# Kernel tuning notes

Hardware: AMD Instinct MI355X
Metric: run time of the kernel (lower is better)

Reference implementation:

```python
import jax, jax.numpy as jnp
import numpy as np

B, V_PREV, V_NEXT = 1, 16384, 65536
F_IN, F_OUT = 512, 256
NNZ_UP, N_EDGE = 65536, 524288
EPS = 1e-5


def batch_spmm(row, col, val, m, x):
    # sparse [m, n] (COO row/col/val) @ dense x [B, n, d] -> [B, m, d]
    contrib = val[None, :, None] * x[:, col, :]          # [B, nnz, d]
    return jnp.zeros((x.shape[0], m, x.shape[2]), x.dtype).at[:, row, :].add(contrib)


def batchnorm(x, g, b):
    # BatchNorm1d in training mode: stats over (batch, node) per channel
    mu = jnp.mean(x, axis=(0, 1), keepdims=True)
    var = jnp.var(x, axis=(0, 1), keepdims=True)
    return (x - mu) * jax.lax.rsqrt(var + EPS) * g + b


def ecc(x, src, dst, w, Ui_W, Ui_b, Uj_W, Uj_b):
    # edge-conditioned graph conv: out_i = Ui(x_i) + sum_{(j->i)} w_e * Uj(x_j)
    n_nodes = x.shape[1]
    uj = x @ Uj_W + Uj_b                                  # [B, V, Fout]
    msg = w[None, :, None] * uj[:, src, :]                # [B, E, Fout]
    agg = jnp.zeros((x.shape[0], n_nodes, Uj_W.shape[1]), x.dtype).at[:, dst, :].add(msg)
    return x @ Ui_W + Ui_b + agg


def setup_inputs() -> dict:
    key = jax.random.key(0)
    ks = jax.random.split(key, 16)
    s_in = 1.0 / np.sqrt(F_IN)
    s_out = 1.0 / np.sqrt(F_OUT)
    p = {}
    p["x"] = jax.random.normal(ks[0], (B, V_PREV, F_IN), jnp.float32)
    p["up_row"] = jnp.arange(NNZ_UP, dtype=jnp.int32)
    p["up_col"] = jax.random.randint(ks[1], (NNZ_UP,), 0, V_PREV)
    p["up_val"] = jax.random.uniform(ks[2], (NNZ_UP,), jnp.float32)
    p["edge_src"] = jax.random.randint(ks[3], (N_EDGE,), 0, V_NEXT)
    p["edge_dst"] = jax.random.randint(ks[4], (N_EDGE,), 0, V_NEXT)
    p["adj_val"] = jax.random.uniform(ks[5], (N_EDGE,), jnp.float32)
    p["W_res"] = jax.random.normal(ks[6], (F_IN, F_OUT), jnp.float32) * s_in
    p["b_res"] = jnp.zeros((F_OUT,), jnp.float32)
    p["bn0_g"] = jnp.ones((F_IN,), jnp.float32)
    p["bn0_b"] = jnp.zeros((F_IN,), jnp.float32)
    p["bn1_g"] = jnp.ones((F_OUT,), jnp.float32)
    p["bn1_b"] = jnp.zeros((F_OUT,), jnp.float32)
    p["Ui0_W"] = jax.random.normal(ks[7], (F_IN, F_OUT), jnp.float32) * s_in
    p["Ui0_b"] = jnp.zeros((F_OUT,), jnp.float32)
    p["Uj0_W"] = jax.random.normal(ks[8], (F_IN, F_OUT), jnp.float32) * s_in
    p["Uj0_b"] = jnp.zeros((F_OUT,), jnp.float32)
    p["Ui1_W"] = jax.random.normal(ks[9], (F_OUT, F_OUT), jnp.float32) * s_out
    p["Ui1_b"] = jnp.zeros((F_OUT,), jnp.float32)
    p["Uj1_W"] = jax.random.normal(ks[10], (F_OUT, F_OUT), jnp.float32) * s_out
    p["Uj1_b"] = jnp.zeros((F_OUT,), jnp.float32)
    return p


def reference(x, up_row, up_col, up_val, edge_src, edge_dst, adj_val,
              W_res, b_res, bn0_g, bn0_b, bn1_g, bn1_b,
              Ui0_W, Ui0_b, Uj0_W, Uj0_b, Ui1_W, Ui1_b, Uj1_W, Uj1_b):
    # residual branch: sparse upsample then 1x1 conv (= linear over channels)
    residual = batch_spmm(up_row, up_col, up_val, V_NEXT, x)      # [B, V_NEXT, F_IN]
    residual = residual @ W_res + b_res                           # [B, V_NEXT, F_OUT]
    # main branch
    out = jax.nn.relu(batchnorm(x, bn0_g, bn0_b))                 # [B, V_PREV, F_IN]
    out = batch_spmm(up_row, up_col, up_val, V_NEXT, out)         # [B, V_NEXT, F_IN]
    out = ecc(out, edge_src, edge_dst, adj_val, Ui0_W, Ui0_b, Uj0_W, Uj0_b)
    out = jax.nn.relu(batchnorm(out, bn1_g, bn1_b))
    out = ecc(out, edge_src, edge_dst, adj_val, Ui1_W, Ui1_b, Uj1_W, Uj1_b)
    return out + residual
```

## Files before the change

kernel.cpp:

```cpp
#include <hip/hip_runtime.h>

#define V_PREV 16384
#define V_NEXT 65536
#define F_IN   512
#define F_OUT  256
#define NNZ_UP 65536
#define N_EDGE 524288

using f32x4 = __attribute__((ext_vector_type(4))) float;
using bfrag = __attribute__((ext_vector_type(8))) short;

__device__ __forceinline__ ushort f2bf(float f) {
    union { float f; unsigned u; } v; v.f = f;
    unsigned r = (v.u + 0x7FFFu + ((v.u >> 16) & 1u)) >> 16;
    return (ushort)r;
}
__device__ __forceinline__ float bf2f(ushort h) {
    union { unsigned u; float f; } v; v.u = ((unsigned)h) << 16; return v.f;
}

__global__ void prep_all_kernel(const float* __restrict__ Wres,
                                const float* __restrict__ Ui0W, const float* __restrict__ Uj0W,
                                const float* __restrict__ Ui1W, const float* __restrict__ Uj1W,
                                const float* __restrict__ Ui1b, const float* __restrict__ bres,
                                const int* __restrict__ up_row, const int* __restrict__ up_col,
                                const float* __restrict__ up_val,
                                ushort* __restrict__ WresT, ushort* __restrict__ W0t,
                                ushort* __restrict__ W1cat, float* __restrict__ biasUi,
                                int* __restrict__ colof, float* __restrict__ valof,
                                int* __restrict__ zeroBase)
{
    int b = blockIdx.x, t = threadIdx.x;
    if (b < 1024) {
        int i = b * 256 + t;
        if (i < 256 * 512) {
            int n = i / 512, k = i % 512;
            WresT[i] = f2bf(Wres[k * 256 + n]);
            W1cat[i] = f2bf(k < 256 ? Ui1W[k * 256 + n] : Uj1W[(k - 256) * 256 + n]);
        }
        {
            int n = i / 512, k = i % 512;
            W0t[i] = f2bf(n < 256 ? Uj0W[k * 256 + n] : Ui0W[k * 256 + (n - 256)]);
        }
        if (i < 256) biasUi[i] = Ui1b[i] + bres[i];
    } else if (b < 1280) {
        int k = (b - 1024) * 256 + t;
        int r = up_row[k];
        colof[r] = up_col[k];
        valof[r] = up_val[k];
    } else {
        int i = (b - 1280) * 256 + t;
        zeroBase[i] = 0;
    }
}

__global__ void hist_bn0_kernel(const int* __restrict__ dst, const float* __restrict__ adjv,
                                int* __restrict__ cnt, float* __restrict__ sumA,
                                const float* __restrict__ x,
                                float* __restrict__ psum0, float* __restrict__ psq0)
{
    int b = blockIdx.x, t = threadIdx.x;
    if (b < 2048) {
        int e = b * 256 + t;
        int d = dst[e];
        atomicAdd(&cnt[d], 1);
        atomicAdd(&sumA[d], adjv[e]);
    } else {
        int blk = b - 2048;
        float s0 = 0, s1 = 0, q0 = 0, q1 = 0;
        for (int r = 0; r < 128; r++) {
            size_t base = ((size_t)blk * 128 + r) * 512;
            float a = x[base + t], bb = x[base + t + 256];
            s0 += a; q0 += a * a; s1 += bb; q1 += bb * bb;
        }
        psum0[blk * 512 + t] = s0; psum0[blk * 512 + t + 256] = s1;
        psq0 [blk * 512 + t] = q0; psq0 [blk * 512 + t + 256] = q1;
    }
}

__global__ void scan_block_kernel(const int* __restrict__ cnt, int* __restrict__ offs,
                                  int* __restrict__ bsum)
{
    __shared__ int buf[2][256];
    int t = threadIdx.x;
    int i = blockIdx.x * 256 + t;
    int v = cnt[i];
    int p = 0;
    buf[0][t] = v;
    __syncthreads();
    for (int d = 1; d < 256; d <<= 1) {
        int nv = buf[p][t] + ((t >= d) ? buf[p][t - d] : 0);
        buf[p ^ 1][t] = nv;
        p ^= 1;
        __syncthreads();
    }
    int incl = buf[p][t];
    offs[i] = incl - v;
    if (t == 255) bsum[blockIdx.x] = incl;
}

__global__ void add_offs_bnfin_kernel(int* __restrict__ offs, const int* __restrict__ bsum,
                                      int* __restrict__ cursor,
                                      const float* __restrict__ psum0, const float* __restrict__ psq0,
                                      const float* __restrict__ g0, const float* __restrict__ b0,
                                      float* __restrict__ sc0, float* __restrict__ sh0)
{
    int b = blockIdx.x, t = threadIdx.x;
    if (b < 256) {
        __shared__ int buf[2][256];
        int v = bsum[t];
        int p = 0;
        buf[0][t] = v;
        __syncthreads();
        for (int d = 1; d < 256; d <<= 1) {
            int nv = buf[p][t] + ((t >= d) ? buf[p][t - d] : 0);
            buf[p ^ 1][t] = nv;
            p ^= 1;
            __syncthreads();
        }
        int excl = buf[p][b] - bsum[b];
        int i = b * 256 + t;
        int o = offs[i] + excl;
        offs[i] = o;
        cursor[i] = o;
    } else {
        int vb = b - 256;
        int gw = (vb * 256 + t) >> 6;
        int lane = t & 63;
        float s = 0, q = 0;
        for (int i = lane; i < 128; i += 64) {
            s += psum0[(size_t)i * 512 + gw];
            q += psq0 [(size_t)i * 512 + gw];
        }
#pragma unroll
        for (int d = 32; d > 0; d >>= 1) {
            s += __shfl_xor(s, d);
            q += __shfl_xor(q, d);
        }
        if (lane == 0) {
            float m = s * (1.0f / V_PREV);
            float v = q * (1.0f / V_PREV) - m * m;
            float r = rsqrtf(v + 1e-5f);
            float scale = r * g0[gw];
            sc0[gw] = scale;
            sh0[gw] = b0[gw] - m * scale;
        }
    }
}

__global__ void fill_kernel(const int* __restrict__ src, const int* __restrict__ dst,
                            const float* __restrict__ adjv,
                            const int* __restrict__ colof, const float* __restrict__ valof,
                            int* __restrict__ cursor,
                            int* __restrict__ srcsA, float* __restrict__ valsA,
                            int* __restrict__ srcs0, float* __restrict__ vals0)
{
    int e = blockIdx.x * blockDim.x + threadIdx.x;
    int d = dst[e];
    int s = src[e];
    float a = adjv[e];
    int p = atomicAdd(&cursor[d], 1);
    srcsA[p] = s;
    valsA[p] = a;
    srcs0[p] = colof[s];
    vals0[p] = a * valof[s];
}

__global__ void bn_finish_kernel(const float* __restrict__ psum, const float* __restrict__ psq,
                                 int nblocks, int C, float invN,
                                 const float* __restrict__ g, const float* __restrict__ b,
                                 float* __restrict__ sc, float* __restrict__ sh)
{
    int gw = (blockIdx.x * blockDim.x + threadIdx.x) >> 6;
    int lane = threadIdx.x & 63;
    if (gw >= C) return;
    float s = 0, q = 0;
    for (int i = lane; i < nblocks; i += 64) {
        s += psum[(size_t)i * C + gw];
        q += psq [(size_t)i * C + gw];
    }
#pragma unroll
    for (int d = 32; d > 0; d >>= 1) {
        s += __shfl_xor(s, d);
        q += __shfl_xor(q, d);
    }
    if (lane == 0) {
        float m = s * invN;
        float v = q * invN - m * m;
        float r = rsqrtf(v + 1e-5f);
        float scale = r * g[gw];
        sc[gw] = scale;
        sh[gw] = b[gw] - m * scale;
    }
}

__global__ __launch_bounds__(256)
void gemm0_fused_kernel(const float* __restrict__ x,
                        const ushort* __restrict__ WresT, const ushort* __restrict__ W0t,
                        const float* __restrict__ sc0, const float* __restrict__ sh0,
                        ushort* __restrict__ XW, ushort* __restrict__ XNJ,
                        ushort* __restrict__ XNI)
{
    __shared__ ushort As[128 * 32];
    __shared__ ushort Bs[128 * 32];
    __shared__ float s_sc[512], s_sh[512];

    const int tid = threadIdx.x;
    const int id   = blockIdx.x;
    const int xcd  = id & 7;
    const int rest = id >> 3;
    const int slot = rest / 6;
    const int bx   = rest - slot * 6;
    const int by   = slot * 8 + xcd;

    const bool bnmode = bx >= 2;
    const ushort* Bt = bnmode ? W0t : WresT;
    const int btrow = bnmode ? (bx - 2) * 128 : bx * 128;
    ushort* Cout = (bx < 2) ? XW : (bx < 4 ? XNJ : XNI);
    const int colbase = (bx & 1) * 128;
    const int tM = by * 128;

    for (int i = tid; i < 512; i += 256) { s_sc[i] = sc0[i]; s_sh[i] = sh0[i]; }
    __syncthreads();

    const int lane = tid & 63;
    const int wave = tid >> 6;
    const int wm = wave >> 1, wn = wave & 1;
    const int lr = lane & 15, lg = lane >> 4;

    const int ra = tid >> 1;
    const int ua = (tid & 1) * 2;
    const int rb = tid >> 2;
    const int ub = tid & 3;

    f32x4 acc[4][4] = {};

    for (int k0 = 0; k0 < 512; k0 += 32) {
        const float* xp = &x[(size_t)(tM + ra) * 512 + k0 + ua * 8];
        float4 f0 = *(const float4*)(xp);
        float4 f1 = *(const float4*)(xp + 4);
        float4 f2 = *(const float4*)(xp + 8);
        float4 f3 = *(const float4*)(xp + 12);
        float vv[16] = { f0.x,f0.y,f0.z,f0.w, f1.x,f1.y,f1.z,f1.w,
                         f2.x,f2.y,f2.z,f2.w, f3.x,f3.y,f3.z,f3.w };
        ushort hh[16];
        if (bnmode) {
#pragma unroll
            for (int j = 0; j < 16; j++) {
                int c = k0 + ua * 8 + j;
                hh[j] = f2bf(fmaxf(vv[j] * s_sc[c] + s_sh[c], 0.0f));
            }
        } else {
#pragma unroll
            for (int j = 0; j < 16; j++) hh[j] = f2bf(vv[j]);
        }
        *(uint4*)&As[ra * 32 + ((ua    ) ^ (ra & 3)) * 8] = *(uint4*)&hh[0];
        *(uint4*)&As[ra * 32 + ((ua + 1) ^ (ra & 3)) * 8] = *(uint4*)&hh[8];

#pragma unroll
        for (int i = 0; i < 2; i++) {
            int row = rb + i * 64;
            *(uint4*)&Bs[row * 32 + (ub ^ (row & 3)) * 8] =
                *(const uint4*)&Bt[(size_t)(btrow + row) * 512 + k0 + ub * 8];
        }
        __syncthreads();

        bfrag af[4], bfv[4];
#pragma unroll
        for (int mm = 0; mm < 4; mm++) {
            int row = wm * 64 + mm * 16 + lr;
            af[mm] = *(const bfrag*)&As[row * 32 + (lg ^ (row & 3)) * 8];
        }
#pragma unroll
        for (int nn = 0; nn < 4; nn++) {
            int row = wn * 64 + nn * 16 + lr;
            bfv[nn] = *(const bfrag*)&Bs[row * 32 + (lg ^ (row & 3)) * 8];
        }
#pragma unroll
        for (int mm = 0; mm < 4; mm++)
#pragma unroll
            for (int nn = 0; nn < 4; nn++)
                acc[mm][nn] = __builtin_amdgcn_mfma_f32_16x16x32_bf16(af[mm], bfv[nn], acc[mm][nn], 0, 0, 0);
        __syncthreads();
    }

#pragma unroll
    for (int mm = 0; mm < 4; mm++)
#pragma unroll
        for (int nn = 0; nn < 4; nn++)
#pragma unroll
            for (int r = 0; r < 4; r++) {
                int row = tM + wm * 64 + mm * 16 + lg * 4 + r;
                int col = colbase + wn * 64 + nn * 16 + lr;
                Cout[(size_t)row * 256 + col] = f2bf(acc[mm][nn][r]);
            }
}

__global__ __launch_bounds__(256)
void gather0_kernel(const int* __restrict__ offs, const int* __restrict__ cnt,
                    const int* __restrict__ srcs0, const float* __restrict__ vals0,
                    const int* __restrict__ colof, const float* __restrict__ valof,
                    const float* __restrict__ sumA,
                    const ushort* __restrict__ XNJ, const ushort* __restrict__ XNI,
                    const float* __restrict__ ui_b, const float* __restrict__ uj_b,
                    ushort* __restrict__ X1,
                    float* __restrict__ psum1s, float* __restrict__ psq1s)
{
    __shared__ float redS[4][256];
    __shared__ float redQ[4][256];

    int wave = threadIdx.x >> 6;
    int f = (threadIdx.x & 63) * 4;
    float ub0 = ui_b[f + 0], ub1 = ui_b[f + 1], ub2 = ui_b[f + 2], ub3 = ui_b[f + 3];
    float jb0 = uj_b[f + 0], jb1 = uj_b[f + 1], jb2 = uj_b[f + 2], jb3 = uj_b[f + 3];
    float ss0 = 0, ss1 = 0, ss2 = 0, ss3 = 0;
    float qq0 = 0, qq1 = 0, qq2 = 0, qq3 = 0;

    for (int it = 0; it < 8; it++) {
        int d = (blockIdx.x * 8 + it) * 4 + wave;
        int c = colof[d];
        float s = valof[d];
        float sA = sumA[d];
        ushort4 u = *(const ushort4*)&XNI[(size_t)c * 256 + f];
        const ushort* up = (const ushort*)&u;
        float a0 = ub0 + sA * jb0 + s * bf2f(up[0]);
        float a1 = ub1 + sA * jb1 + s * bf2f(up[1]);
        float a2 = ub2 + sA * jb2 + s * bf2f(up[2]);
        float a3 = ub3 + sA * jb3 + s * bf2f(up[3]);

        int st = offs[d], n = cnt[d];
        for (int e0 = 0; e0 < n; e0 += 4) {
            int   i0 = srcs0[st + e0];
            float w0 = vals0[st + e0];
            int i1 = 0, i2 = 0, i3 = 0;
            float w1 = 0, w2 = 0, w3 = 0;
            if (e0 + 1 < n) { i1 = srcs0[st + e0 + 1]; w1 = vals0[st + e0 + 1]; }
            if (e0 + 2 < n) { i2 = srcs0[st + e0 + 2]; w2 = vals0[st + e0 + 2]; }
            if (e0 + 3 < n) { i3 = srcs0[st + e0 + 3]; w3 = vals0[st + e0 + 3]; }
            ushort4 v0 = *(const ushort4*)&XNJ[(size_t)i0 * 256 + f];
            ushort4 v1 = *(const ushort4*)&XNJ[(size_t)i1 * 256 + f];
            ushort4 v2 = *(const ushort4*)&XNJ[(size_t)i2 * 256 + f];
            ushort4 v3 = *(const ushort4*)&XNJ[(size_t)i3 * 256 + f];
            const ushort* p0 = (const ushort*)&v0;
            const ushort* p1 = (const ushort*)&v1;
            const ushort* p2 = (const ushort*)&v2;
            const ushort* p3 = (const ushort*)&v3;
            a0 += w0 * bf2f(p0[0]) + w1 * bf2f(p1[0]) + w2 * bf2f(p2[0]) + w3 * bf2f(p3[0]);
            a1 += w0 * bf2f(p0[1]) + w1 * bf2f(p1[1]) + w2 * bf2f(p2[1]) + w3 * bf2f(p3[1]);
            a2 += w0 * bf2f(p0[2]) + w1 * bf2f(p1[2]) + w2 * bf2f(p2[2]) + w3 * bf2f(p3[2]);
            a3 += w0 * bf2f(p0[3]) + w1 * bf2f(p1[3]) + w2 * bf2f(p2[3]) + w3 * bf2f(p3[3]);
        }
        *(ushort4*)&X1[(size_t)d * 256 + f] =
            make_ushort4(f2bf(a0), f2bf(a1), f2bf(a2), f2bf(a3));
        ss0 += a0; ss1 += a1; ss2 += a2; ss3 += a3;
        qq0 += a0 * a0; qq1 += a1 * a1; qq2 += a2 * a2; qq3 += a3 * a3;
    }

    redS[wave][f + 0] = ss0; redS[wave][f + 1] = ss1;
    redS[wave][f + 2] = ss2; redS[wave][f + 3] = ss3;
    redQ[wave][f + 0] = qq0; redQ[wave][f + 1] = qq1;
    redQ[wave][f + 2] = qq2; redQ[wave][f + 3] = qq3;
    __syncthreads();
    int t = threadIdx.x;
    float ssum = redS[0][t] + redS[1][t] + redS[2][t] + redS[3][t];
    float sq   = redQ[0][t] + redQ[1][t] + redQ[2][t] + redQ[3][t];
    int slab = (blockIdx.x & 63) * 256 + t;
    atomicAdd(&psum1s[slab], ssum);
    atomicAdd(&psq1s[slab], sq);
}

__global__ __launch_bounds__(256)
void gather1G_kernel(const int* __restrict__ offs, const int* __restrict__ cnt,
                     const int* __restrict__ srcsA, const float* __restrict__ valsA,
                     const ushort* __restrict__ X1,
                     const float* __restrict__ sc1, const float* __restrict__ sh1,
                     ushort* __restrict__ G)
{
    int d = blockIdx.x * 4 + (threadIdx.x >> 6);
    int f = (threadIdx.x & 63) * 4;
    float4 sc = *(const float4*)&sc1[f];
    float4 sh = *(const float4*)&sh1[f];
    float a0 = 0, a1 = 0, a2 = 0, a3 = 0;

    int st = offs[d], n = cnt[d];
    for (int e0 = 0; e0 < n; e0 += 4) {
        int   i0 = srcsA[st + e0];
        float w0 = valsA[st + e0];
        int i1 = 0, i2 = 0, i3 = 0;
        float w1 = 0, w2 = 0, w3 = 0;
        if (e0 + 1 < n) { i1 = srcsA[st + e0 + 1]; w1 = valsA[st + e0 + 1]; }
        if (e0 + 2 < n) { i2 = srcsA[st + e0 + 2]; w2 = valsA[st + e0 + 2]; }
        if (e0 + 3 < n) { i3 = srcsA[st + e0 + 3]; w3 = valsA[st + e0 + 3]; }
        ushort4 v0 = *(const ushort4*)&X1[(size_t)i0 * 256 + f];
        ushort4 v1 = *(const ushort4*)&X1[(size_t)i1 * 256 + f];
        ushort4 v2 = *(const ushort4*)&X1[(size_t)i2 * 256 + f];
        ushort4 v3 = *(const ushort4*)&X1[(size_t)i3 * 256 + f];
        const ushort* p0 = (const ushort*)&v0;
        const ushort* p1 = (const ushort*)&v1;
        const ushort* p2 = (const ushort*)&v2;
        const ushort* p3 = (const ushort*)&v3;
        a0 += w0 * fmaxf(bf2f(p0[0]) * sc.x + sh.x, 0.0f)
            + w1 * fmaxf(bf2f(p1[0]) * sc.x + sh.x, 0.0f)
            + w2 * fmaxf(bf2f(p2[0]) * sc.x + sh.x, 0.0f)
            + w3 * fmaxf(bf2f(p3[0]) * sc.x + sh.x, 0.0f);
        a1 += w0 * fmaxf(bf2f(p0[1]) * sc.y + sh.y, 0.0f)
            + w1 * fmaxf(bf2f(p1[1]) * sc.y + sh.y, 0.0f)
            + w2 * fmaxf(bf2f(p2[1]) * sc.y + sh.y, 0.0f)
            + w3 * fmaxf(bf2f(p3[1]) * sc.y + sh.y, 0.0f);
        a2 += w0 * fmaxf(bf2f(p0[2]) * sc.z + sh.z, 0.0f)
            + w1 * fmaxf(bf2f(p1[2]) * sc.z + sh.z, 0.0f)
            + w2 * fmaxf(bf2f(p2[2]) * sc.z + sh.z, 0.0f)
            + w3 * fmaxf(bf2f(p3[2]) * sc.z + sh.z, 0.0f);
        a3 += w0 * fmaxf(bf2f(p0[3]) * sc.w + sh.w, 0.0f)
            + w1 * fmaxf(bf2f(p1[3]) * sc.w + sh.w, 0.0f)
            + w2 * fmaxf(bf2f(p2[3]) * sc.w + sh.w, 0.0f)
            + w3 * fmaxf(bf2f(p3[3]) * sc.w + sh.w, 0.0f);
    }
    *(ushort4*)&G[(size_t)d * 256 + f] =
        make_ushort4(f2bf(a0), f2bf(a1), f2bf(a2), f2bf(a3));
}

__global__ __launch_bounds__(512, 1)
void gemm_final_kernel(const ushort* __restrict__ X1, const ushort* __restrict__ G,
                       const ushort* __restrict__ W1cat,
                       const float* __restrict__ sc1, const float* __restrict__ sh1,
                       const float* __restrict__ biasUi, const float* __restrict__ uj1_b,
                       const float* __restrict__ sumA,
                       const int* __restrict__ colof, const float* __restrict__ valof,
                       const ushort* __restrict__ XW,
                       float* __restrict__ out)
{
    __shared__ ushort As[256 * 32];
    __shared__ ushort Bs[256 * 32];
    __shared__ float s_sc[256], s_sh[256];

    const int tid = threadIdx.x;
    const int tM = blockIdx.x * 256;

    if (tid < 256) { s_sc[tid] = sc1[tid]; s_sh[tid] = sh1[tid]; }
    __syncthreads();

    const int lane = tid & 63;
    const int wave = tid >> 6;
    const int wm = wave >> 1, wn = wave & 1;
    const int lr = lane & 15, lg = lane >> 4;

    f32x4 acc[4][8] = {};

    for (int k0 = 0; k0 < 512; k0 += 32) {
#pragma unroll
        for (int i = 0; i < 2; i++) {
            int idx = tid + i * 512;
            int row = idx >> 2, u = idx & 3;
            ushort h[8];
            if (k0 < 256) {
                *(uint4*)h = *(const uint4*)&X1[(size_t)(tM + row) * 256 + k0 + u * 8];
#pragma unroll
                for (int j = 0; j < 8; j++) {
                    int c = k0 + u * 8 + j;
                    h[j] = f2bf(fmaxf(bf2f(h[j]) * s_sc[c] + s_sh[c], 0.0f));
                }
            } else {
                *(uint4*)h = *(const uint4*)&G[(size_t)(tM + row) * 256 + (k0 - 256) + u * 8];
            }
            *(uint4*)&As[row * 32 + (u ^ (row & 3)) * 8] = *(uint4*)h;
        }
#pragma unroll
        for (int i = 0; i < 2; i++) {
            int idx = tid + i * 512;
            int row = idx >> 2, u = idx & 3;
            *(uint4*)&Bs[row * 32 + (u ^ (row & 3)) * 8] =
                *(const uint4*)&W1cat[(size_t)row * 512 + k0 + u * 8];
        }
        __syncthreads();

        bfrag af[4], bfv[8];
#pragma unroll
        for (int mm = 0; mm < 4; mm++) {
            int row = wm * 64 + mm * 16 + lr;
            af[mm] = *(const bfrag*)&As[row * 32 + (lg ^ (row & 3)) * 8];
        }
#pragma unroll
        for (int nn = 0; nn < 8; nn++) {
            int row = wn * 128 + nn * 16 + lr;
            bfv[nn] = *(const bfrag*)&Bs[row * 32 + (lg ^ (row & 3)) * 8];
        }
#pragma unroll
        for (int mm = 0; mm < 4; mm++)
#pragma unroll
            for (int nn = 0; nn < 8; nn++)
                acc[mm][nn] = __builtin_amdgcn_mfma_f32_16x16x32_bf16(af[mm], bfv[nn], acc[mm][nn], 0, 0, 0);
        __syncthreads();
    }

    float bUi[8], bUj[8];
#pragma unroll
    for (int nn = 0; nn < 8; nn++) {
        int col = wn * 128 + nn * 16 + lr;
        bUi[nn] = biasUi[col];
        bUj[nn] = uj1_b[col];
    }
#pragma unroll
    for (int mm = 0; mm < 4; mm++) {
#pragma unroll
        for (int r = 0; r < 4; r++) {
            int row = tM + wm * 64 + mm * 16 + lg * 4 + r;
            int c = colof[row];
            float s = valof[row];
            float sA = sumA[row];
#pragma unroll
            for (int nn = 0; nn < 8; nn++) {
                int col = wn * 128 + nn * 16 + lr;
                float v = acc[mm][nn][r] + bUi[nn] + sA * bUj[nn]
                        + s * bf2f(XW[(size_t)c * 256 + col]);
                out[(size_t)row * 256 + col] = v;
            }
        }
    }
}

extern "C" void kernel_launch(void* const* d_in, const int* in_sizes, int n_in,
                              void* d_out, int out_size, void* d_ws, size_t ws_size,
                              hipStream_t stream)
{
    const float* x      = (const float*)d_in[0];
    const int*   up_row = (const int*)  d_in[1];
    const int*   up_col = (const int*)  d_in[2];
    const float* up_val = (const float*)d_in[3];
    const int*   e_src  = (const int*)  d_in[4];
    const int*   e_dst  = (const int*)  d_in[5];
    const float* adjv   = (const float*)d_in[6];
    const float* W_res  = (const float*)d_in[7];
    const float* b_res  = (const float*)d_in[8];
    const float* bn0_g  = (const float*)d_in[9];
    const float* bn0_b  = (const float*)d_in[10];
    const float* bn1_g  = (const float*)d_in[11];
    const float* bn1_b  = (const float*)d_in[12];
    const float* Ui0_W  = (const float*)d_in[13];
    const float* Ui0_b  = (const float*)d_in[14];
    const float* Uj0_W  = (const float*)d_in[15];
    const float* Uj0_b  = (const float*)d_in[16];
    const float* Ui1_W  = (const float*)d_in[17];
    const float* Ui1_b  = (const float*)d_in[18];
    const float* Uj1_W  = (const float*)d_in[19];
    const float* Uj1_b  = (const float*)d_in[20];

    float* out = (float*)d_out;

    char* ws = (char*)d_ws;
    size_t off = 0;
    auto alloc = [&](size_t bytes) -> char* {
        char* p = ws + off;
        off = (off + bytes + 255) & ~(size_t)255;
        return p;
    };
    ushort* XW    = (ushort*)alloc((size_t)V_PREV * F_OUT * 2);
    ushort* XNJ   = (ushort*)alloc((size_t)V_PREV * F_OUT * 2);
    ushort* XNI   = (ushort*)alloc((size_t)V_PREV * F_OUT * 2);
    ushort* X1    = (ushort*)alloc((size_t)V_NEXT * F_OUT * 2);
    ushort* G     = (ushort*)alloc((size_t)V_NEXT * F_OUT * 2);
    int*    cnt   = (int*)   alloc(V_NEXT * 4);
    float*  sumA  = (float*) alloc(V_NEXT * 4);
    float*  psum1s= (float*) alloc(64 * 256 * 4);
    float*  psq1s = (float*) alloc(64 * 256 * 4);
    int*    offs  = (int*)   alloc(V_NEXT * 4);
    int*    cursor= (int*)   alloc(V_NEXT * 4);
    int*    bsum  = (int*)   alloc(256 * 4);
    int*    srcsA = (int*)   alloc((size_t)N_EDGE * 4);
    float*  valsA = (float*) alloc((size_t)N_EDGE * 4);
    int*    srcs0 = (int*)   alloc((size_t)N_EDGE * 4);
    float*  vals0 = (float*) alloc((size_t)N_EDGE * 4);
    int*    colof = (int*)   alloc(V_NEXT * 4);
    float*  valof = (float*) alloc(V_NEXT * 4);
    ushort* WresT = (ushort*)alloc(256 * 512 * 2);
    ushort* W0t   = (ushort*)alloc(512 * 512 * 2);
    ushort* W1cat = (ushort*)alloc(256 * 512 * 2);
    float*  biasUi= (float*) alloc(256 * 4);
    float*  psum0 = (float*) alloc(128 * 512 * 4);
    float*  psq0  = (float*) alloc(128 * 512 * 4);
    float*  sc0   = (float*) alloc(512 * 4);
    float*  sh0   = (float*) alloc(512 * 4);
    float*  sc1   = (float*) alloc(256 * 4);
    float*  sh1   = (float*) alloc(256 * 4);
    (void)ws_size; (void)in_sizes; (void)n_in; (void)out_size;

    prep_all_kernel<<<1920, 256, 0, stream>>>(W_res, Ui0_W, Uj0_W, Ui1_W, Uj1_W,
                                              Ui1_b, b_res,
                                              up_row, up_col, up_val,
                                              WresT, W0t, W1cat, biasUi,
                                              colof, valof, cnt);

    hist_bn0_kernel<<<2176, 256, 0, stream>>>(e_dst, adjv, cnt, sumA, x, psum0, psq0);

    scan_block_kernel<<<256, 256, 0, stream>>>(cnt, offs, bsum);

    add_offs_bnfin_kernel<<<384, 256, 0, stream>>>(offs, bsum, cursor,
                                                   psum0, psq0, bn0_g, bn0_b, sc0, sh0);

    fill_kernel<<<N_EDGE / 256, 256, 0, stream>>>(e_src, e_dst, adjv, colof, valof,
                                                  cursor, srcsA, valsA, srcs0, vals0);

    gemm0_fused_kernel<<<768, 256, 0, stream>>>(x, WresT, W0t, sc0, sh0, XW, XNJ, XNI);

    gather0_kernel<<<2048, 256, 0, stream>>>(offs, cnt, srcs0, vals0,
                                             colof, valof, sumA,
                                             XNJ, XNI, Ui0_b, Uj0_b, X1,
                                             psum1s, psq1s);

    bn_finish_kernel<<<64, 256, 0, stream>>>(psum1s, psq1s, 64, 256, 1.0f / V_NEXT,
                                             bn1_g, bn1_b, sc1, sh1);

    gather1G_kernel<<<V_NEXT / 4, 256, 0, stream>>>(offs, cnt, srcsA, valsA,
                                                    X1, sc1, sh1, G);

    gemm_final_kernel<<<256, 512, 0, stream>>>(X1, G, W1cat, sc1, sh1,
                                               biasUi, Uj1_b, sumA,
                                               colof, valof, XW, out);
}
```

Measured before the change: 274.3 us.

## Pack edge arrays into int4, fuse fill into GEMM0, compute sumA in gather

Merges the four per-edge arrays (src, adj weight, upsampled src, combined weight) into one int4 record per edge, so each gather does a single 16-byte load instead of separate scalar loads. The CSR fill is folded into the GEMM0 launch as extra blocks, which removes a kernel boundary and lets the fill overlap with the matrix multiply. The per-destination sumA float atomics are dropped from the histogram and sumA is instead summed inside gather0 from the edge records. The BN0 partial-sum pass is also split into more, smaller blocks. Costs are a wider record that gather1 reads in full while using only half, and a fill-then-GEMM ordering inside one grid.

```diff
diff --git a/kernel.cpp b/kernel.cpp
--- a/kernel.cpp
+++ b/kernel.cpp
@@ -54,22 +54,20 @@
     }
 }
 
-__global__ void hist_bn0_kernel(const int* __restrict__ dst, const float* __restrict__ adjv,
-                                int* __restrict__ cnt, float* __restrict__ sumA,
+__global__ void hist_bn0_kernel(const int* __restrict__ dst,
+                                int* __restrict__ cnt,
                                 const float* __restrict__ x,
                                 float* __restrict__ psum0, float* __restrict__ psq0)
 {
     int b = blockIdx.x, t = threadIdx.x;
     if (b < 2048) {
         int e = b * 256 + t;
-        int d = dst[e];
-        atomicAdd(&cnt[d], 1);
-        atomicAdd(&sumA[d], adjv[e]);
+        atomicAdd(&cnt[dst[e]], 1);
     } else {
         int blk = b - 2048;
         float s0 = 0, s1 = 0, q0 = 0, q1 = 0;
-        for (int r = 0; r < 128; r++) {
-            size_t base = ((size_t)blk * 128 + r) * 512;
+        for (int r = 0; r < 32; r++) {
+            size_t base = ((size_t)blk * 32 + r) * 512;
             float a = x[base + t], bb = x[base + t + 256];
             s0 += a; q0 += a * a; s1 += bb; q1 += bb * bb;
         }
@@ -128,7 +126,7 @@
         int gw = (vb * 256 + t) >> 6;
         int lane = t & 63;
         float s = 0, q = 0;
-        for (int i = lane; i < 128; i += 64) {
+        for (int i = lane; i < 512; i += 64) {
             s += psum0[(size_t)i * 512 + gw];
             q += psq0 [(size_t)i * 512 + gw];
         }
@@ -148,24 +146,6 @@
     }
 }
 
-__global__ void fill_kernel(const int* __restrict__ src, const int* __restrict__ dst,
-                            const float* __restrict__ adjv,
-                            const int* __restrict__ colof, const float* __restrict__ valof,
-                            int* __restrict__ cursor,
-                            int* __restrict__ srcsA, float* __restrict__ valsA,
-                            int* __restrict__ srcs0, float* __restrict__ vals0)
-{
-    int e = blockIdx.x * blockDim.x + threadIdx.x;
-    int d = dst[e];
-    int s = src[e];
-    float a = adjv[e];
-    int p = atomicAdd(&cursor[d], 1);
-    srcsA[p] = s;
-    valsA[p] = a;
-    srcs0[p] = colof[s];
-    vals0[p] = a * valof[s];
-}
-
 __global__ void bn_finish_kernel(const float* __restrict__ psum, const float* __restrict__ psq,
                                  int nblocks, int C, float invN,
                                  const float* __restrict__ g, const float* __restrict__ b,
@@ -195,18 +175,37 @@
 }
 
 __global__ __launch_bounds__(256)
-void gemm0_fused_kernel(const float* __restrict__ x,
-                        const ushort* __restrict__ WresT, const ushort* __restrict__ W0t,
-                        const float* __restrict__ sc0, const float* __restrict__ sh0,
-                        ushort* __restrict__ XW, ushort* __restrict__ XNJ,
-                        ushort* __restrict__ XNI)
+void fill_gemm0_kernel(const int* __restrict__ src, const int* __restrict__ dst,
+                       const float* __restrict__ adjv,
+                       const int* __restrict__ colof, const float* __restrict__ valof,
+                       int* __restrict__ cursor, int4* __restrict__ E,
+                       const float* __restrict__ x,
+                       const ushort* __restrict__ WresT, const ushort* __restrict__ W0t,
+                       const float* __restrict__ sc0, const float* __restrict__ sh0,
+                       ushort* __restrict__ XW, ushort* __restrict__ XNJ,
+                       ushort* __restrict__ XNI)
 {
     __shared__ ushort As[128 * 32];
     __shared__ ushort Bs[128 * 32];
     __shared__ float s_sc[512], s_sh[512];
 
     const int tid = threadIdx.x;
-    const int id   = blockIdx.x;
+    if (blockIdx.x < 2048) {
+        int e = blockIdx.x * 256 + tid;
+        int d = dst[e];
+        int s = src[e];
+        float a = adjv[e];
+        int p = atomicAdd(&cursor[d], 1);
+        int4 v;
+        v.x = s;
+        v.y = __float_as_int(a);
+        v.z = colof[s];
+        v.w = __float_as_int(a * valof[s]);
+        E[p] = v;
+        return;
+    }
+
+    const int id   = blockIdx.x - 2048;
     const int xcd  = id & 7;
     const int rest = id >> 3;
     const int slot = rest / 6;
@@ -298,19 +297,19 @@
 
 __global__ __launch_bounds__(256)
 void gather0_kernel(const int* __restrict__ offs, const int* __restrict__ cnt,
-                    const int* __restrict__ srcs0, const float* __restrict__ vals0,
+                    const int4* __restrict__ E,
                     const int* __restrict__ colof, const float* __restrict__ valof,
-                    const float* __restrict__ sumA,
                     const ushort* __restrict__ XNJ, const ushort* __restrict__ XNI,
                     const float* __restrict__ ui_b, const float* __restrict__ uj_b,
-                    ushort* __restrict__ X1,
+                    ushort* __restrict__ X1, float* __restrict__ sumA,
                     float* __restrict__ psum1s, float* __restrict__ psq1s)
 {
     __shared__ float redS[4][256];
     __shared__ float redQ[4][256];
 
     int wave = threadIdx.x >> 6;
-    int f = (threadIdx.x & 63) * 4;
+    int lane = threadIdx.x & 63;
+    int f = lane * 4;
     float ub0 = ui_b[f + 0], ub1 = ui_b[f + 1], ub2 = ui_b[f + 2], ub3 = ui_b[f + 3];
     float jb0 = uj_b[f + 0], jb1 = uj_b[f + 1], jb2 = uj_b[f + 2], jb3 = uj_b[f + 3];
     float ss0 = 0, ss1 = 0, ss2 = 0, ss3 = 0;
@@ -320,27 +319,28 @@
         int d = (blockIdx.x * 8 + it) * 4 + wave;
         int c = colof[d];
         float s = valof[d];
-        float sA = sumA[d];
         ushort4 u = *(const ushort4*)&XNI[(size_t)c * 256 + f];
         const ushort* up = (const ushort*)&u;
-        float a0 = ub0 + sA * jb0 + s * bf2f(up[0]);
-        float a1 = ub1 + sA * jb1 + s * bf2f(up[1]);
-        float a2 = ub2 + sA * jb2 + s * bf2f(up[2]);
-        float a3 = ub3 + sA * jb3 + s * bf2f(up[3]);
+        float a0 = ub0 + s * bf2f(up[0]);
+        float a1 = ub1 + s * bf2f(up[1]);
+        float a2 = ub2 + s * bf2f(up[2]);
+        float a3 = ub3 + s * bf2f(up[3]);
+        float sA = 0;
 
         int st = offs[d], n = cnt[d];
         for (int e0 = 0; e0 < n; e0 += 4) {
-            int   i0 = srcs0[st + e0];
-            float w0 = vals0[st + e0];
-            int i1 = 0, i2 = 0, i3 = 0;
-            float w1 = 0, w2 = 0, w3 = 0;
-            if (e0 + 1 < n) { i1 = srcs0[st + e0 + 1]; w1 = vals0[st + e0 + 1]; }
-            if (e0 + 2 < n) { i2 = srcs0[st + e0 + 2]; w2 = vals0[st + e0 + 2]; }
-            if (e0 + 3 < n) { i3 = srcs0[st + e0 + 3]; w3 = vals0[st + e0 + 3]; }
-            ushort4 v0 = *(const ushort4*)&XNJ[(size_t)i0 * 256 + f];
-            ushort4 v1 = *(const ushort4*)&XNJ[(size_t)i1 * 256 + f];
-            ushort4 v2 = *(const ushort4*)&XNJ[(size_t)i2 * 256 + f];
-            ushort4 v3 = *(const ushort4*)&XNJ[(size_t)i3 * 256 + f];
+            int4 ev0 = E[st + e0];
+            int4 ev1 = (e0 + 1 < n) ? E[st + e0 + 1] : make_int4(0, 0, 0, 0);
+            int4 ev2 = (e0 + 2 < n) ? E[st + e0 + 2] : make_int4(0, 0, 0, 0);
+            int4 ev3 = (e0 + 3 < n) ? E[st + e0 + 3] : make_int4(0, 0, 0, 0);
+            float w0 = __int_as_float(ev0.w), w1 = __int_as_float(ev1.w);
+            float w2 = __int_as_float(ev2.w), w3 = __int_as_float(ev3.w);
+            sA += __int_as_float(ev0.y) + __int_as_float(ev1.y)
+                + __int_as_float(ev2.y) + __int_as_float(ev3.y);
+            ushort4 v0 = *(const ushort4*)&XNJ[(size_t)ev0.z * 256 + f];
+            ushort4 v1 = *(const ushort4*)&XNJ[(size_t)ev1.z * 256 + f];
+            ushort4 v2 = *(const ushort4*)&XNJ[(size_t)ev2.z * 256 + f];
+            ushort4 v3 = *(const ushort4*)&XNJ[(size_t)ev3.z * 256 + f];
             const ushort* p0 = (const ushort*)&v0;
             const ushort* p1 = (const ushort*)&v1;
             const ushort* p2 = (const ushort*)&v2;
@@ -350,8 +350,10 @@
             a2 += w0 * bf2f(p0[2]) + w1 * bf2f(p1[2]) + w2 * bf2f(p2[2]) + w3 * bf2f(p3[2]);
             a3 += w0 * bf2f(p0[3]) + w1 * bf2f(p1[3]) + w2 * bf2f(p2[3]) + w3 * bf2f(p3[3]);
         }
+        a0 += sA * jb0; a1 += sA * jb1; a2 += sA * jb2; a3 += sA * jb3;
         *(ushort4*)&X1[(size_t)d * 256 + f] =
             make_ushort4(f2bf(a0), f2bf(a1), f2bf(a2), f2bf(a3));
+        if (lane == 0) sumA[d] = sA;
         ss0 += a0; ss1 += a1; ss2 += a2; ss3 += a3;
         qq0 += a0 * a0; qq1 += a1 * a1; qq2 += a2 * a2; qq3 += a3 * a3;
     }
@@ -371,7 +373,7 @@
 
 __global__ __launch_bounds__(256)
 void gather1G_kernel(const int* __restrict__ offs, const int* __restrict__ cnt,
-                     const int* __restrict__ srcsA, const float* __restrict__ valsA,
+                     const int4* __restrict__ E,
                      const ushort* __restrict__ X1,
                      const float* __restrict__ sc1, const float* __restrict__ sh1,
                      ushort* __restrict__ G)
@@ -384,17 +386,16 @@
 
     int st = offs[d], n = cnt[d];
     for (int e0 = 0; e0 < n; e0 += 4) {
-        int   i0 = srcsA[st + e0];
-        float w0 = valsA[st + e0];
-        int i1 = 0, i2 = 0, i3 = 0;
-        float w1 = 0, w2 = 0, w3 = 0;
-        if (e0 + 1 < n) { i1 = srcsA[st + e0 + 1]; w1 = valsA[st + e0 + 1]; }
-        if (e0 + 2 < n) { i2 = srcsA[st + e0 + 2]; w2 = valsA[st + e0 + 2]; }
-        if (e0 + 3 < n) { i3 = srcsA[st + e0 + 3]; w3 = valsA[st + e0 + 3]; }
-        ushort4 v0 = *(const ushort4*)&X1[(size_t)i0 * 256 + f];
-        ushort4 v1 = *(const ushort4*)&X1[(size_t)i1 * 256 + f];
-        ushort4 v2 = *(const ushort4*)&X1[(size_t)i2 * 256 + f];
-        ushort4 v3 = *(const ushort4*)&X1[(size_t)i3 * 256 + f];
+        int4 ev0 = E[st + e0];
+        int4 ev1 = (e0 + 1 < n) ? E[st + e0 + 1] : make_int4(0, 0, 0, 0);
+        int4 ev2 = (e0 + 2 < n) ? E[st + e0 + 2] : make_int4(0, 0, 0, 0);
+        int4 ev3 = (e0 + 3 < n) ? E[st + e0 + 3] : make_int4(0, 0, 0, 0);
+        float w0 = __int_as_float(ev0.y), w1 = __int_as_float(ev1.y);
+        float w2 = __int_as_float(ev2.y), w3 = __int_as_float(ev3.y);
+        ushort4 v0 = *(const ushort4*)&X1[(size_t)ev0.x * 256 + f];
+        ushort4 v1 = *(const ushort4*)&X1[(size_t)ev1.x * 256 + f];
+        ushort4 v2 = *(const ushort4*)&X1[(size_t)ev2.x * 256 + f];
+        ushort4 v3 = *(const ushort4*)&X1[(size_t)ev3.x * 256 + f];
         const ushort* p0 = (const ushort*)&v0;
         const ushort* p1 = (const ushort*)&v1;
         const ushort* p2 = (const ushort*)&v2;
@@ -560,58 +561,53 @@
     ushort* X1    = (ushort*)alloc((size_t)V_NEXT * F_OUT * 2);
     ushort* G     = (ushort*)alloc((size_t)V_NEXT * F_OUT * 2);
     int*    cnt   = (int*)   alloc(V_NEXT * 4);
-    float*  sumA  = (float*) alloc(V_NEXT * 4);
     float*  psum1s= (float*) alloc(64 * 256 * 4);
     float*  psq1s = (float*) alloc(64 * 256 * 4);
+    float*  sumA  = (float*) alloc(V_NEXT * 4);
     int*    offs  = (int*)   alloc(V_NEXT * 4);
     int*    cursor= (int*)   alloc(V_NEXT * 4);
     int*    bsum  = (int*)   alloc(256 * 4);
-    int*    srcsA = (int*)   alloc((size_t)N_EDGE * 4);
-    float*  valsA = (float*) alloc((size_t)N_EDGE * 4);
-    int*    srcs0 = (int*)   alloc((size_t)N_EDGE * 4);
-    float*  vals0 = (float*) alloc((size_t)N_EDGE * 4);
+    int4*   E     = (int4*)  alloc((size_t)N_EDGE * 16);
     int*    colof = (int*)   alloc(V_NEXT * 4);
     float*  valof = (float*) alloc(V_NEXT * 4);
     ushort* WresT = (ushort*)alloc(256 * 512 * 2);
     ushort* W0t   = (ushort*)alloc(512 * 512 * 2);
     ushort* W1cat = (ushort*)alloc(256 * 512 * 2);
     float*  biasUi= (float*) alloc(256 * 4);
-    float*  psum0 = (float*) alloc(128 * 512 * 4);
-    float*  psq0  = (float*) alloc(128 * 512 * 4);
+    float*  psum0 = (float*) alloc(512 * 512 * 4);
+    float*  psq0  = (float*) alloc(512 * 512 * 4);
     float*  sc0   = (float*) alloc(512 * 4);
     float*  sh0   = (float*) alloc(512 * 4);
     float*  sc1   = (float*) alloc(256 * 4);
     float*  sh1   = (float*) alloc(256 * 4);
     (void)ws_size; (void)in_sizes; (void)n_in; (void)out_size;
 
-    prep_all_kernel<<<1920, 256, 0, stream>>>(W_res, Ui0_W, Uj0_W, Ui1_W, Uj1_W,
+    prep_all_kernel<<<1664, 256, 0, stream>>>(W_res, Ui0_W, Uj0_W, Ui1_W, Uj1_W,
                                               Ui1_b, b_res,
                                               up_row, up_col, up_val,
                                               WresT, W0t, W1cat, biasUi,
                                               colof, valof, cnt);
 
-    hist_bn0_kernel<<<2176, 256, 0, stream>>>(e_dst, adjv, cnt, sumA, x, psum0, psq0);
+    hist_bn0_kernel<<<2560, 256, 0, stream>>>(e_dst, cnt, x, psum0, psq0);
 
     scan_block_kernel<<<256, 256, 0, stream>>>(cnt, offs, bsum);
 
     add_offs_bnfin_kernel<<<384, 256, 0, stream>>>(offs, bsum, cursor,
                                                    psum0, psq0, bn0_g, bn0_b, sc0, sh0);
 
-    fill_kernel<<<N_EDGE / 256, 256, 0, stream>>>(e_src, e_dst, adjv, colof, valof,
-                                                  cursor, srcsA, valsA, srcs0, vals0);
-
-    gemm0_fused_kernel<<<768, 256, 0, stream>>>(x, WresT, W0t, sc0, sh0, XW, XNJ, XNI);
-
-    gather0_kernel<<<2048, 256, 0, stream>>>(offs, cnt, srcs0, vals0,
-                                             colof, valof, sumA,
-                                             XNJ, XNI, Ui0_b, Uj0_b, X1,
-                                             psum1s, psq1s);
+    fill_gemm0_kernel<<<2816, 256, 0, stream>>>(e_src, e_dst, adjv, colof, valof,
+                                                cursor, E,
+                                                x, WresT, W0t, sc0, sh0,
+                                                XW, XNJ, XNI);
+
+    gather0_kernel<<<2048, 256, 0, stream>>>(offs, cnt, E, colof, valof,
+                                             XNJ, XNI, Ui0_b, Uj0_b,
+                                             X1, sumA, psum1s, psq1s);
 
     bn_finish_kernel<<<64, 256, 0, stream>>>(psum1s, psq1s, 64, 256, 1.0f / V_NEXT,
                                              bn1_g, bn1_b, sc1, sh1);
 
-    gather1G_kernel<<<V_NEXT / 4, 256, 0, stream>>>(offs, cnt, srcsA, valsA,
-                                                    X1, sc1, sh1, G);
+    gather1G_kernel<<<V_NEXT / 4, 256, 0, stream>>>(offs, cnt, E, X1, sc1, sh1, G);
 
     gemm_final_kernel<<<256, 512, 0, stream>>>(X1, G, W1cat, sc1, sh1,
                                                biasUi, Uj1_b, sumA,
```

Measured after the change: 238.1 us. 13.2% less time.
